# Optimization experiments

Measured on AMD Instinct MI355X. Metric: run time of the kernel, lower is better.

## Reference

```python
import jax, jax.numpy as jnp
import numpy as np

WINDOWS = (3, 5, 7)
B, L, D = 8, 512, 768
NUM_LABELS = 9


def setup_inputs() -> dict:
    key = jax.random.key(0)
    ks = jax.random.split(key, 7)
    n = len(WINDOWS)
    return {
        "sequence_output": jax.random.normal(ks[0], (B, L, D), jnp.float32),
        "W_ih": jax.random.normal(ks[1], (n, 4 * D, D), jnp.float32) * 0.02,
        "W_hh": jax.random.normal(ks[2], (n, 4 * D, D), jnp.float32) * 0.02,
        "b_ih": jax.random.normal(ks[3], (n, 4 * D), jnp.float32) * 0.02,
        "b_hh": jax.random.normal(ks[4], (n, 4 * D), jnp.float32) * 0.02,
        "lin_w": jax.random.normal(ks[5], (NUM_LABELS, D), jnp.float32) * 0.02,
        "lin_b": jnp.zeros((NUM_LABELS,), jnp.float32),
    }


def _windowed_lstm(x, w, Wih, Whh, bih, bhh):
    # Vectorized equivalent of windows_sequence: for each position i, run an
    # LSTM over the sorted in-range neighborhood of radius w//2 around i and
    # take the final hidden state (state after the rightmost valid token).
    Bb, Ll, Dd = x.shape
    h = w // 2
    offs = jnp.arange(-h, h + 1)                      # [W]
    pos = jnp.arange(Ll)[:, None] + offs[None, :]     # [L, W]
    valid = (pos >= 0) & (pos < Ll)                   # [L, W]
    idx = jnp.clip(pos, 0, Ll - 1)
    win = x[:, idx, :]                                # [B, L, W, D]
    xs = jnp.moveaxis(win, 2, 0)                      # [W, B, L, D] scan axis first
    vs = valid.T                                      # [W, L]

    def step(carry, inp):
        hs, cs = carry                                # [B, L, D] each
        x_t, v_t = inp                                # [B, L, D], [L]
        gates = x_t @ Wih.T + bih + hs @ Whh.T + bhh  # [B, L, 4D]; torch gate order i,f,g,o
        i, f, g, o = jnp.split(gates, 4, axis=-1)
        i = jax.nn.sigmoid(i)
        f = jax.nn.sigmoid(f)
        g = jnp.tanh(g)
        o = jax.nn.sigmoid(o)
        c_new = f * cs + i * g
        h_new = o * jnp.tanh(c_new)
        m = v_t[None, :, None]                        # skip out-of-range window slots
        return (jnp.where(m, h_new, hs), jnp.where(m, c_new, cs)), None

    init = (jnp.zeros_like(x), jnp.zeros_like(x))
    (h_fin, _), _ = jax.lax.scan(step, init, (xs, vs))
    return h_fin                                      # [B, L, D]


def reference(sequence_output, W_ih, W_hh, b_ih, b_hh, lin_w, lin_b):
    x = sequence_output
    # one short LSTM scan per window size (small fixed set)
    locals_ = jnp.stack(
        [_windowed_lstm(x, w, W_ih[k], W_hh[k], b_ih[k], b_hh[k])
         for k, w in enumerate(WINDOWS)], axis=2)     # [B, L, n_win, D]
    d_k = x.shape[-1]
    attn = jnp.einsum('bld,blnd->bln', x, locals_) / jnp.sqrt(jnp.float32(d_k))
    attn = jax.nn.softmax(attn, axis=-1)
    local_features = jnp.einsum('bln,blnd->bld', attn, locals_)
    out = x + local_features
    return out @ lin_w.T + lin_b                      # [B, L, num_labels]
```

## Files before the change

kernel.cpp:

```cpp
#include <hip/hip_runtime.h>
#include <math.h>

#define BB   8
#define LL   512
#define DD   768
#define G4   3072
#define NW   3
#define NLAB 9
#define MM   4096

typedef unsigned short u16;
typedef __attribute__((ext_vector_type(8))) __bf16 bf16x8;
typedef __attribute__((ext_vector_type(4))) float  f32x4;

#define AS1 __attribute__((address_space(1)))
#define AS3 __attribute__((address_space(3)))

#define OFF_G    ((size_t)0)
#define OFF_C    ((size_t)150994944)
#define OFF_H    ((size_t)188743680)
#define OFF_XB   ((size_t)226492416)
#define OFF_WIHB ((size_t)232783872)
#define OFF_WHHB ((size_t)246939648)

__device__ __forceinline__ float sigm(float x) { return 1.0f / (1.0f + expf(-x)); }

__device__ __forceinline__ u16 f2bf(float f) {
    union { float f; unsigned u; } v; v.f = f;
    unsigned r = v.u + 0x7FFFu + ((v.u >> 16) & 1u);
    return (u16)(r >> 16);
}
__device__ __forceinline__ float bf2f(u16 h) {
    union { unsigned u; float f; } v; v.u = ((unsigned)h) << 16;
    return v.f;
}

__global__ __launch_bounds__(256)
void k_cvt(const float* __restrict__ in, u16* __restrict__ out, int n4)
{
    int i = blockIdx.x * 256 + threadIdx.x;
    if (i >= n4) return;
    float4 v = reinterpret_cast<const float4*>(in)[i];
    ushort4 o;
    o.x = f2bf(v.x); o.y = f2bf(v.y); o.z = f2bf(v.z); o.w = f2bf(v.w);
    reinterpret_cast<ushort4*>(out)[i] = o;
}

template<int MODE>
__global__ __launch_bounds__(256)
void k_mfma(const u16* __restrict__ Ab,
            const u16* __restrict__ Wb,
            const float* __restrict__ bih,
            const float* __restrict__ bhh,
            float* __restrict__ Gbuf,
            u16* __restrict__ hnext,
            float* __restrict__ cbuf,
            int kmin, int s)
{
    const int k    = kmin + blockIdx.z;
    const int r0   = blockIdx.x * 128;
    const int tid  = threadIdx.x;
    const int lane = tid & 63;
    const int wid  = tid >> 6;
    const int wm   = wid >> 1, wn = wid & 1;

    __shared__ bf16x8 As[1024];
    __shared__ bf16x8 Bs[1024];

    const u16* Asrc = (MODE == 0) ? Ab : (Ab + (size_t)k * MM * DD);
    const u16* Wk   = Wb + (size_t)k * G4 * DD;

    const int l3 = lane >> 3;
    const int l7 = lane & 7;
    const int sg = l7 ^ l3;
    const u16* gA[4]; const u16* gB[4];
#pragma unroll
    for (int i = 0; i < 4; ++i) {
        int chunk = wid * 4 + i;
        int rowA  = chunk * 8 + l3;
        gA[i] = Asrc + (size_t)(r0 + rowA) * DD + sg * 8;
        int p = chunk * 8 + l3;
        int j;
        if (MODE == 0) {
            j = blockIdx.y * 128 + p;
        } else {
            int cell = (p & 15) + 16 * (p >> 6);
            int g    = (p >> 4) & 3;
            j = g * DD + blockIdx.y * 32 + cell;
        }
        gB[i] = Wk + (size_t)j * DD + sg * 8;
    }

    f32x4 acc[4][4];
#pragma unroll
    for (int a = 0; a < 4; ++a)
#pragma unroll
        for (int b = 0; b < 4; ++b) acc[a][b] = (f32x4)0.0f;

    const int c15 = lane & 15;
    const int khi = lane >> 4;

    for (int k0 = 0; k0 < DD; k0 += 64) {
#pragma unroll
        for (int i = 0; i < 4; ++i) {
            __builtin_amdgcn_global_load_lds(
                (const AS1 void*)(gA[i] + k0),
                (AS3 void*)((char*)As + (wid * 4 + i) * 1024), 16, 0, 0);
            __builtin_amdgcn_global_load_lds(
                (const AS1 void*)(gB[i] + k0),
                (AS3 void*)((char*)Bs + (wid * 4 + i) * 1024), 16, 0, 0);
        }
        __syncthreads();

#pragma unroll
        for (int ks = 0; ks < 2; ++ks) {
            bf16x8 af[4], bfr[4];
#pragma unroll
            for (int mi = 0; mi < 4; ++mi) {
                int row  = wm * 64 + mi * 16 + c15;
                int slot = (ks * 4 + khi) ^ (row & 7);
                af[mi] = As[row * 8 + slot];
            }
#pragma unroll
            for (int ni = 0; ni < 4; ++ni) {
                int row  = wn * 64 + ni * 16 + c15;
                int slot = (ks * 4 + khi) ^ (row & 7);
                bfr[ni] = Bs[row * 8 + slot];
            }
#pragma unroll
            for (int mi = 0; mi < 4; ++mi)
#pragma unroll
                for (int ni = 0; ni < 4; ++ni)
                    acc[mi][ni] = __builtin_amdgcn_mfma_f32_16x16x32_bf16(
                        af[mi], bfr[ni], acc[mi][ni], 0, 0, 0);
        }
        __syncthreads();
    }

    if (MODE == 0) {
        float* Gk = Gbuf + (size_t)k * MM * G4;
        const int j0 = blockIdx.y * 128;
#pragma unroll
        for (int ni = 0; ni < 4; ++ni) {
            int j = j0 + wn * 64 + ni * 16 + c15;
            float bsum = bih[k * G4 + j] + bhh[k * G4 + j];
#pragma unroll
            for (int mi = 0; mi < 4; ++mi)
#pragma unroll
                for (int q = 0; q < 4; ++q) {
                    int r = r0 + wm * 64 + mi * 16 + khi * 4 + q;
                    Gk[(size_t)r * G4 + j] = acc[mi][ni][q] + bsum;
                }
        }
    } else {
        const float* Gk = Gbuf + (size_t)k * MM * G4;
        u16*  hn = hnext + (size_t)k * MM * DD;
        const u16* hp = Asrc;
        float* ck = cbuf + (size_t)k * MM * DD;
        const int n  = blockIdx.y * 32 + wn * 16 + c15;
        const int hw = k + 1;
#pragma unroll
        for (int mi = 0; mi < 4; ++mi)
#pragma unroll
            for (int q = 0; q < 4; ++q) {
                int r = r0 + wm * 64 + mi * 16 + khi * 4 + q;
                int l = r & (LL - 1);
                int pos = l - hw + s;
                bool valid = (pos >= 0) && (pos < LL);
                int posc = min(max(pos, 0), LL - 1);
                size_t rowG = (size_t)(r - l + posc) * G4;
                float gi = sigm (acc[mi][0][q] + Gk[rowG + 0 * DD + n]);
                float gf = sigm (acc[mi][1][q] + Gk[rowG + 1 * DD + n]);
                float gg = tanhf(acc[mi][2][q] + Gk[rowG + 2 * DD + n]);
                float go = sigm (acc[mi][3][q] + Gk[rowG + 3 * DD + n]);
                size_t off = (size_t)r * DD + n;
                if (valid) {
                    float cold = ck[off];
                    float cnew = gf * cold + gi * gg;
                    ck[off] = cnew;
                    hn[off] = f2bf(go * tanhf(cnew));
                } else {
                    hn[off] = hp[off];
                }
            }
    }
}

__global__ __launch_bounds__(256)
void k_init(const float* __restrict__ G, u16* __restrict__ h0,
            float* __restrict__ c0)
{
    int idx = blockIdx.x * 256 + threadIdx.x;
    int k   = idx / (MM * DD);
    int rem = idx - k * (MM * DD);
    int r   = rem / DD;
    int n   = rem - r * DD;
    int l   = r & (LL - 1);
    int hw  = k + 1;
    int pos = l - hw;
    bool valid = (pos >= 0);
    int posc = valid ? pos : 0;
    const float* Grow = G + (size_t)k * MM * G4 + (size_t)(r - l + posc) * G4 + n;
    float gi = sigm (Grow[0 * DD]);
    float gg = tanhf(Grow[2 * DD]);
    float go = sigm (Grow[3 * DD]);
    float cn = gi * gg;
    float hv = go * tanhf(cn);
    size_t off = (size_t)k * MM * DD + (size_t)r * DD + n;
    h0[off] = valid ? f2bf(hv) : (u16)0;
    c0[off] = valid ? cn : 0.0f;
}

__global__ __launch_bounds__(256)
void k_final(const float* __restrict__ x, const u16* __restrict__ hfin,
             const float* __restrict__ linw, const float* __restrict__ linb,
             float* __restrict__ out)
{
    int wave = threadIdx.x >> 6, lane = threadIdx.x & 63;
    int r = blockIdx.x * 4 + wave;
    const float* xr = x + (size_t)r * DD;
    const u16* h0 = hfin + (size_t)0 * MM * DD + (size_t)r * DD;
    const u16* h1 = hfin + (size_t)1 * MM * DD + (size_t)r * DD;
    const u16* h2 = hfin + (size_t)2 * MM * DD + (size_t)r * DD;

    float xe[12], he0[12], he1[12], he2[12];
    float s0 = 0.f, s1 = 0.f, s2 = 0.f;
#pragma unroll
    for (int q = 0; q < 12; ++q) {
        int e = lane + 64 * q;
        xe[q] = xr[e];
        he0[q] = bf2f(h0[e]); he1[q] = bf2f(h1[e]); he2[q] = bf2f(h2[e]);
        s0 = fmaf(xe[q], he0[q], s0);
        s1 = fmaf(xe[q], he1[q], s1);
        s2 = fmaf(xe[q], he2[q], s2);
    }
#pragma unroll
    for (int d = 1; d < 64; d <<= 1) {
        s0 += __shfl_xor(s0, d, 64);
        s1 += __shfl_xor(s1, d, 64);
        s2 += __shfl_xor(s2, d, 64);
    }
    const float scale = 0.03608439182435161f;
    s0 *= scale; s1 *= scale; s2 *= scale;
    float mx = fmaxf(s0, fmaxf(s1, s2));
    float e0 = expf(s0 - mx), e1 = expf(s1 - mx), e2 = expf(s2 - mx);
    float inv = 1.0f / (e0 + e1 + e2);
    float a0 = e0 * inv, a1 = e1 * inv, a2 = e2 * inv;

    float p[9];
#pragma unroll
    for (int j = 0; j < 9; ++j) p[j] = 0.0f;
#pragma unroll
    for (int q = 0; q < 12; ++q) {
        int e = lane + 64 * q;
        float o = xe[q] + a0 * he0[q] + a1 * he1[q] + a2 * he2[q];
#pragma unroll
        for (int j = 0; j < 9; ++j)
            p[j] = fmaf(o, linw[j * DD + e], p[j]);
    }
#pragma unroll
    for (int j = 0; j < 9; ++j)
#pragma unroll
        for (int d = 1; d < 64; d <<= 1)
            p[j] += __shfl_xor(p[j], d, 64);
    if (lane == 0) {
#pragma unroll
        for (int j = 0; j < 9; ++j)
            out[(size_t)r * NLAB + j] = p[j] + linb[j];
    }
}

extern "C" void kernel_launch(void* const* d_in, const int* in_sizes, int n_in,
                              void* d_out, int out_size, void* d_ws, size_t ws_size,
                              hipStream_t stream)
{
    const float* x    = (const float*)d_in[0];
    const float* Wih  = (const float*)d_in[1];
    const float* Whh  = (const float*)d_in[2];
    const float* bih  = (const float*)d_in[3];
    const float* bhh  = (const float*)d_in[4];
    const float* linw = (const float*)d_in[5];
    const float* linb = (const float*)d_in[6];
    float* out = (float*)d_out;
    char*  ws  = (char*)d_ws;

    float* G    = (float*)(ws + OFF_G);
    float* C    = (float*)(ws + OFF_C);
    u16*   H    = (u16*)  (ws + OFF_H);
    u16*   xb   = (u16*)  (ws + OFF_XB);
    u16*   Wihb = (u16*)  (ws + OFF_WIHB);
    u16*   Whhb = (u16*)  (ws + OFF_WHHB);

    dim3 blk(256);

    k_cvt<<<(MM * DD / 4 + 255) / 256, blk, 0, stream>>>(x, xb, MM * DD / 4);
    k_cvt<<<(NW * G4 * DD / 4 + 255) / 256, blk, 0, stream>>>(Wih, Wihb, NW * G4 * DD / 4);
    k_cvt<<<(NW * G4 * DD / 4 + 255) / 256, blk, 0, stream>>>(Whh, Whhb, NW * G4 * DD / 4);

    k_mfma<0><<<dim3(32, 24, 3), blk, 0, stream>>>(
        xb, Wihb, bih, bhh, G, nullptr, nullptr, 0, 0);

    k_init<<<(NW * MM * DD) / 256, blk, 0, stream>>>(G, H, C);

    for (int s = 1; s < 7; ++s) {
        int kmin = (s < 3) ? 0 : ((s < 5) ? 1 : 2);
        int nact = 3 - kmin;
        u16* hprev = H + (size_t)((s - 1) & 1) * NW * MM * DD;
        u16* hnx   = H + (size_t)(s & 1) * NW * MM * DD;
        k_mfma<1><<<dim3(32, 24, nact), blk, 0, stream>>>(
            hprev, Whhb, nullptr, nullptr, G, hnx, C, kmin, s);
    }

    k_final<<<MM / 4, blk, 0, stream>>>(x, H, linw, linb, out);
}
```

Baseline: 796.0 us.

## Store input-gate projections as packed bf16 and fuse LSTM init into GEMM

The input-projection GEMM now stores the four gate preactivations per cell as packed bf16 ushort4 instead of an fp32 [rows,3072] buffer, which halves G traffic and turns the recurrent step's four strided loads into one vector load. The separate init kernel is removed: the MODE 0 epilogue computes the first LSTM step, scattering h0/c0 to the shifted row r+hw. The three conversion launches are merged into one. Storing gate preactivations in bf16 loses precision, and the scattered epilogue writes may coalesce poorly.

```diff
diff --git a/kernel.cpp b/kernel.cpp
--- a/kernel.cpp
+++ b/kernel.cpp
@@ -17,11 +17,11 @@
 #define AS3 __attribute__((address_space(3)))
 
 #define OFF_G    ((size_t)0)
-#define OFF_C    ((size_t)150994944)
-#define OFF_H    ((size_t)188743680)
-#define OFF_XB   ((size_t)226492416)
-#define OFF_WIHB ((size_t)232783872)
-#define OFF_WHHB ((size_t)246939648)
+#define OFF_C    ((size_t)75497472)
+#define OFF_H    ((size_t)113246208)
+#define OFF_XB   ((size_t)150994944)
+#define OFF_WIHB ((size_t)157286400)
+#define OFF_WHHB ((size_t)171442176)
 
 __device__ __forceinline__ float sigm(float x) { return 1.0f / (1.0f + expf(-x)); }
 
@@ -36,14 +36,21 @@
 }
 
 __global__ __launch_bounds__(256)
-void k_cvt(const float* __restrict__ in, u16* __restrict__ out, int n4)
+void k_cvt3(const float* __restrict__ a, const float* __restrict__ b,
+            const float* __restrict__ c,
+            u16* __restrict__ oa, u16* __restrict__ ob, u16* __restrict__ oc,
+            int na4, int nb4, int nc4)
 {
     int i = blockIdx.x * 256 + threadIdx.x;
-    if (i >= n4) return;
-    float4 v = reinterpret_cast<const float4*>(in)[i];
+    const float* src; u16* dst; int j;
+    if (i < na4)                  { src = a; dst = oa; j = i; }
+    else if (i < na4 + nb4)       { src = b; dst = ob; j = i - na4; }
+    else if (i < na4 + nb4 + nc4) { src = c; dst = oc; j = i - na4 - nb4; }
+    else return;
+    float4 v = reinterpret_cast<const float4*>(src)[j];
     ushort4 o;
     o.x = f2bf(v.x); o.y = f2bf(v.y); o.z = f2bf(v.z); o.w = f2bf(v.w);
-    reinterpret_cast<ushort4*>(out)[i] = o;
+    reinterpret_cast<ushort4*>(dst)[j] = o;
 }
 
 template<int MODE>
@@ -52,7 +59,7 @@
             const u16* __restrict__ Wb,
             const float* __restrict__ bih,
             const float* __restrict__ bhh,
-            float* __restrict__ Gbuf,
+            u16* __restrict__ Gp,
             u16* __restrict__ hnext,
             float* __restrict__ cbuf,
             int kmin, int s)
@@ -79,15 +86,10 @@
         int chunk = wid * 4 + i;
         int rowA  = chunk * 8 + l3;
         gA[i] = Asrc + (size_t)(r0 + rowA) * DD + sg * 8;
-        int p = chunk * 8 + l3;
-        int j;
-        if (MODE == 0) {
-            j = blockIdx.y * 128 + p;
-        } else {
-            int cell = (p & 15) + 16 * (p >> 6);
-            int g    = (p >> 4) & 3;
-            j = g * DD + blockIdx.y * 32 + cell;
-        }
+        int p    = chunk * 8 + l3;
+        int cell = (p & 15) + 16 * (p >> 6);
+        int g    = (p >> 4) & 3;
+        int j    = g * DD + blockIdx.y * 32 + cell;
         gB[i] = Wk + (size_t)j * DD + sg * 8;
     }
 
@@ -137,28 +139,44 @@
         __syncthreads();
     }
 
+    const int n  = blockIdx.y * 32 + wn * 16 + c15;
+    const int hw = k + 1;
+
     if (MODE == 0) {
-        float* Gk = Gbuf + (size_t)k * MM * G4;
-        const int j0 = blockIdx.y * 128;
-#pragma unroll
-        for (int ni = 0; ni < 4; ++ni) {
-            int j = j0 + wn * 64 + ni * 16 + c15;
-            float bsum = bih[k * G4 + j] + bhh[k * G4 + j];
-#pragma unroll
-            for (int mi = 0; mi < 4; ++mi)
-#pragma unroll
-                for (int q = 0; q < 4; ++q) {
-                    int r = r0 + wm * 64 + mi * 16 + khi * 4 + q;
-                    Gk[(size_t)r * G4 + j] = acc[mi][ni][q] + bsum;
-                }
-        }
+        u16*   Gk = Gp    + ((size_t)k * MM * DD) * 4;
+        u16*   h0 = hnext + (size_t)k * MM * DD;
+        float* c0 = cbuf  + (size_t)k * MM * DD;
+        const float bs0 = bih[k * G4 + 0 * DD + n] + bhh[k * G4 + 0 * DD + n];
+        const float bs1 = bih[k * G4 + 1 * DD + n] + bhh[k * G4 + 1 * DD + n];
+        const float bs2 = bih[k * G4 + 2 * DD + n] + bhh[k * G4 + 2 * DD + n];
+        const float bs3 = bih[k * G4 + 3 * DD + n] + bhh[k * G4 + 3 * DD + n];
+#pragma unroll
+        for (int mi = 0; mi < 4; ++mi)
+#pragma unroll
+            for (int q = 0; q < 4; ++q) {
+                int r = r0 + wm * 64 + mi * 16 + khi * 4 + q;
+                float p0 = acc[mi][0][q] + bs0;
+                float p1 = acc[mi][1][q] + bs1;
+                float p2 = acc[mi][2][q] + bs2;
+                float p3 = acc[mi][3][q] + bs3;
+                ushort4 pk;
+                pk.x = f2bf(p0); pk.y = f2bf(p1); pk.z = f2bf(p2); pk.w = f2bf(p3);
+                *reinterpret_cast<ushort4*>(Gk + ((size_t)r * DD + n) * 4) = pk;
+                int l  = r & (LL - 1);
+                bool ok = (l + hw) < LL;
+                int rt = ok ? (r + hw) : (r + hw - LL);
+                float iv = sigm(p0), gv = tanhf(p2), ov = sigm(p3);
+                float cn = iv * gv;
+                float hv = ov * tanhf(cn);
+                size_t offt = (size_t)rt * DD + n;
+                c0[offt] = ok ? cn : 0.0f;
+                h0[offt] = ok ? f2bf(hv) : (u16)0;
+            }
     } else {
-        const float* Gk = Gbuf + (size_t)k * MM * G4;
+        const u16* Gk = Gp + ((size_t)k * MM * DD) * 4;
         u16*  hn = hnext + (size_t)k * MM * DD;
         const u16* hp = Asrc;
         float* ck = cbuf + (size_t)k * MM * DD;
-        const int n  = blockIdx.y * 32 + wn * 16 + c15;
-        const int hw = k + 1;
 #pragma unroll
         for (int mi = 0; mi < 4; ++mi)
 #pragma unroll
@@ -168,11 +186,12 @@
                 int pos = l - hw + s;
                 bool valid = (pos >= 0) && (pos < LL);
                 int posc = min(max(pos, 0), LL - 1);
-                size_t rowG = (size_t)(r - l + posc) * G4;
-                float gi = sigm (acc[mi][0][q] + Gk[rowG + 0 * DD + n]);
-                float gf = sigm (acc[mi][1][q] + Gk[rowG + 1 * DD + n]);
-                float gg = tanhf(acc[mi][2][q] + Gk[rowG + 2 * DD + n]);
-                float go = sigm (acc[mi][3][q] + Gk[rowG + 3 * DD + n]);
+                ushort4 g4 = *reinterpret_cast<const ushort4*>(
+                    Gk + ((size_t)(r - l + posc) * DD + n) * 4);
+                float gi = sigm (acc[mi][0][q] + bf2f(g4.x));
+                float gf = sigm (acc[mi][1][q] + bf2f(g4.y));
+                float gg = tanhf(acc[mi][2][q] + bf2f(g4.z));
+                float go = sigm (acc[mi][3][q] + bf2f(g4.w));
                 size_t off = (size_t)r * DD + n;
                 if (valid) {
                     float cold = ck[off];
@@ -184,31 +203,6 @@
                 }
             }
     }
-}
-
-__global__ __launch_bounds__(256)
-void k_init(const float* __restrict__ G, u16* __restrict__ h0,
-            float* __restrict__ c0)
-{
-    int idx = blockIdx.x * 256 + threadIdx.x;
-    int k   = idx / (MM * DD);
-    int rem = idx - k * (MM * DD);
-    int r   = rem / DD;
-    int n   = rem - r * DD;
-    int l   = r & (LL - 1);
-    int hw  = k + 1;
-    int pos = l - hw;
-    bool valid = (pos >= 0);
-    int posc = valid ? pos : 0;
-    const float* Grow = G + (size_t)k * MM * G4 + (size_t)(r - l + posc) * G4 + n;
-    float gi = sigm (Grow[0 * DD]);
-    float gg = tanhf(Grow[2 * DD]);
-    float go = sigm (Grow[3 * DD]);
-    float cn = gi * gg;
-    float hv = go * tanhf(cn);
-    size_t off = (size_t)k * MM * DD + (size_t)r * DD + n;
-    h0[off] = valid ? f2bf(hv) : (u16)0;
-    c0[off] = valid ? cn : 0.0f;
 }
 
 __global__ __launch_bounds__(256)
@@ -284,7 +278,7 @@
     float* out = (float*)d_out;
     char*  ws  = (char*)d_ws;
 
-    float* G    = (float*)(ws + OFF_G);
+    u16*   Gp   = (u16*)  (ws + OFF_G);
     float* C    = (float*)(ws + OFF_C);
     u16*   H    = (u16*)  (ws + OFF_H);
     u16*   xb   = (u16*)  (ws + OFF_XB);
@@ -293,14 +287,13 @@
 
     dim3 blk(256);
 
-    k_cvt<<<(MM * DD / 4 + 255) / 256, blk, 0, stream>>>(x, xb, MM * DD / 4);
-    k_cvt<<<(NW * G4 * DD / 4 + 255) / 256, blk, 0, stream>>>(Wih, Wihb, NW * G4 * DD / 4);
-    k_cvt<<<(NW * G4 * DD / 4 + 255) / 256, blk, 0, stream>>>(Whh, Whhb, NW * G4 * DD / 4);
+    const int na4 = MM * DD / 4;
+    const int nb4 = NW * G4 * DD / 4;
+    k_cvt3<<<(na4 + 2 * nb4 + 255) / 256, blk, 0, stream>>>(
+        x, Wih, Whh, xb, Wihb, Whhb, na4, nb4, nb4);
 
     k_mfma<0><<<dim3(32, 24, 3), blk, 0, stream>>>(
-        xb, Wihb, bih, bhh, G, nullptr, nullptr, 0, 0);
-
-    k_init<<<(NW * MM * DD) / 256, blk, 0, stream>>>(G, H, C);
+        xb, Wihb, bih, bhh, Gp, H, C, 0, 0);
 
     for (int s = 1; s < 7; ++s) {
         int kmin = (s < 3) ? 0 : ((s < 5) ? 1 : 2);
@@ -308,7 +301,7 @@
         u16* hprev = H + (size_t)((s - 1) & 1) * NW * MM * DD;
         u16* hnx   = H + (size_t)(s & 1) * NW * MM * DD;
         k_mfma<1><<<dim3(32, 24, nact), blk, 0, stream>>>(
-            hprev, Whhb, nullptr, nullptr, G, hnx, C, kmin, s);
+            hprev, Whhb, nullptr, nullptr, Gp, hnx, C, kmin, s);
     }
 
     k_final<<<MM / 4, blk, 0, stream>>>(x, H, linw, linb, out);
```

Measured after the change: 778.1 us. -2.3%, faster.
